# Performance work log

Measured on AMD Instinct MI355X. Metric: run time of the kernel, lower is better.

Reference implementation:

```python
import jax, jax.numpy as jnp
import numpy as np

H, NH, HD = 1024, 16, 64
WIN = 256
W = WIN // 2  # one-sided window
EXP = 4
PAD_VAL = 0.0  # pad_token_id
B, S0 = 2, 2048
NEG = float(np.finfo(np.float32).min)


def setup_inputs() -> dict:
    key = jax.random.key(0)
    ks = jax.random.split(key, 12)

    def lin(k, fi, fo):
        k1, k2 = jax.random.split(k)
        w = jax.random.normal(k1, (fi, fo), jnp.float32) / np.float32(np.sqrt(fi))
        b = jax.random.normal(k2, (fo,), jnp.float32) * 0.02
        return w, b

    x = jax.random.normal(ks[0], (B, S0, H), jnp.float32)
    mask = jnp.zeros((B, S0), jnp.int32)  # 0 = real token, 1 = pad
    wq, bq = lin(ks[1], H, H)
    wk, bk = lin(ks[2], H, H)
    wv, bv = lin(ks[3], H, H)
    wqg, bqg = lin(ks[4], H, H)
    wkg, bkg = lin(ks[5], H, H)
    wvg, bvg = lin(ks[6], H, H)
    ln_g = jnp.ones((H,), jnp.float32)
    ln_b = jnp.zeros((H,), jnp.float32)
    w1, b1 = lin(ks[7], H, H * EXP)
    w2, b2 = lin(ks[8], H * EXP, H)
    return dict(x=x, mask=mask, wq=wq, bq=bq, wk=wk, bk=bk, wv=wv, bv=bv,
                wqg=wqg, bqg=bqg, wkg=wkg, bkg=bkg, wvg=wvg, bvg=bvg,
                ln_g=ln_g, ln_b=ln_b, w1=w1, b1=b1, w2=w2, b2=b2)


def _forward(x, mask, wq, bq, wk, bk, wv, bv, wqg, bqg, wkg, bkg, wvg, bvg,
             ln_g, ln_b, w1, b1, w2, b2):
    Bsz, s0, _ = x.shape
    pad = WIN - s0 % WIN
    xp = jnp.pad(x, ((0, 0), (0, pad), (0, 0)), constant_values=PAD_VAL)
    m = jnp.pad(mask, ((0, 0), (0, pad)), constant_values=1)
    S = s0 + pad
    lm = (m * -10000).at[:, -1].set(10000)  # [B,S]; task='cls': last token global
    is_masked = lm < 0
    remove = lm != 0  # masked OR global keys removed from local windows

    inv_sqrt = np.float32(1.0 / np.sqrt(HD))
    q = ((xp @ wq + bq) * inv_sqrt).reshape(Bsz, S, NH, HD)
    k = (xp @ wk + bk).reshape(Bsz, S, NH, HD)
    v = (xp @ wv + bv).reshape(Bsz, S, NH, HD)

    nc = S // W
    # chunked banded scores: query chunk of W attends to 3W keys (prev/self/next)
    qc = q.transpose(0, 2, 1, 3).reshape(Bsz, NH, nc, W, HD)
    kpad = jnp.pad(k.transpose(0, 2, 1, 3), ((0, 0), (0, 0), (W, W), (0, 0)))
    idx3w = jnp.arange(nc)[:, None] * W + jnp.arange(3 * W)[None, :]  # [nc,3W]
    kc = kpad[:, :, idx3w]  # [B,NH,nc,3W,HD]
    sc = jnp.einsum('bhcpd,bhckd->bhcpk', qc, kc)  # [B,NH,nc,W,3W]
    p_idx = jnp.arange(W)[:, None]
    d_idx = jnp.arange(2 * W + 1)[None, :]
    band = sc[:, :, :, p_idx, p_idx + d_idx]  # [B,NH,nc,W,2W+1]
    band = band.reshape(Bsz, NH, S, 2 * W + 1).transpose(0, 2, 1, 3)  # [B,S,NH,2W+1]

    # key index j = i + d - W for offset d in [0, 2W]
    j = jnp.arange(S)[:, None] + jnp.arange(2 * W + 1)[None, :] - W
    in_range = (j >= 0) & (j < S)
    jc = jnp.clip(j, 0, S - 1)
    fmask = jnp.where(remove, NEG, 0.0)  # [B,S]
    band = band + fmask[:, jc][:, :, None, :]
    band = jnp.where(in_range[None, :, None, :], band, -jnp.inf)

    # global key column (single global token = last position), concatenated in front
    gcol = jnp.einsum('bshd,bhd->bsh', q, k[:, -1])[..., None]  # [B,S,NH,1]
    scores = jnp.concatenate([gcol, band], axis=-1)  # [B,S,NH,2W+2]
    probs = jax.nn.softmax(scores, axis=-1)
    probs = jnp.where(is_masked[:, :, None, None], 0.0, probs)

    out_g = probs[..., 0][..., None] * v[:, -1][:, None]  # [B,S,NH,HD]
    lp = probs[..., 1:].transpose(0, 2, 1, 3).reshape(Bsz, NH, nc, W, 2 * W + 1)
    pc = jnp.zeros((Bsz, NH, nc, W, 3 * W), probs.dtype).at[:, :, :, p_idx, p_idx + d_idx].set(lp)
    vpad = jnp.pad(v.transpose(0, 2, 1, 3), ((0, 0), (0, 0), (W, W), (0, 0)))
    vc = vpad[:, :, idx3w]  # [B,NH,nc,3W,HD]
    out_l = jnp.einsum('bhcpk,bhckd->bhcpd', pc, vc).reshape(Bsz, NH, S, HD).transpose(0, 2, 1, 3)
    attn = (out_l + out_g).reshape(Bsz, S, H)

    # full global attention for the global token (separate projections)
    qg = ((xp[:, -1] @ wqg + bqg) * inv_sqrt).reshape(Bsz, NH, HD)
    kg = (xp @ wkg + bkg).reshape(Bsz, S, NH, HD)
    vg = (xp @ wvg + bvg).reshape(Bsz, S, NH, HD)
    gs = jnp.einsum('bhd,bshd->bhs', qg, kg)
    gs = jnp.where(is_masked[:, None, :], NEG, gs)
    gout = jnp.einsum('bhs,bshd->bhd', jax.nn.softmax(gs, axis=-1), vg).reshape(Bsz, H)
    attn = attn.at[:, -1].set(gout)

    y = (xp + attn)[:, :s0]  # residual then strip padding
    mu = y.mean(-1, keepdims=True)
    var = ((y - mu) ** 2).mean(-1, keepdims=True)
    y = (y - mu) * jax.lax.rsqrt(var + 1e-5) * ln_g + ln_b
    h = jax.nn.gelu(y @ w1 + b1, approximate=False)
    return y + (h @ w2 + b2)


def reference(x, mask, wq, bq, wk, bk, wv, bv, wqg, bqg, wkg, bkg, wvg, bvg,
              ln_g, ln_b, w1, b1, w2, b2):
    return _forward(x, mask, wq, bq, wk, bk, wv, bv, wqg, bqg, wkg, bkg,
                    wvg, bvg, ln_g, ln_b, w1, b1, w2, b2)
```

## Files before the change

kernel.cpp:

```cpp
#include <hip/hip_runtime.h>


using bf16x8 = __attribute__((ext_vector_type(8))) short;
using bf16x4 = __attribute__((ext_vector_type(4))) short;
using f32x4  = __attribute__((ext_vector_type(4))) float;

__device__ __forceinline__ float b2f(short s) {
    return __uint_as_float(((unsigned int)(unsigned short)s) << 16);
}
__device__ __forceinline__ short f2b(float f) {
    unsigned int u = __float_as_uint(f);
    u += 0x7fffu + ((u >> 16) & 1u);
    return (short)(u >> 16);
}
__device__ __forceinline__ f32x4 mfma16(bf16x8 a, bf16x8 b, f32x4 c) {
    return __builtin_amdgcn_mfma_f32_16x16x32_bf16(a, b, c, 0, 0, 0);
}
__device__ __forceinline__ float safe_exp(float x) {
    return expf((x <= 0.f) ? x : 0.f);
}
__device__ __forceinline__ float fast_gelu(float v) {
    float z  = fabsf(v) * 0.70710678118f;
    float t  = __builtin_amdgcn_rcpf(fmaf(0.47047f, z, 1.f));
    float e  = __expf(-z * z);
    float p  = t * fmaf(t, fmaf(t, 0.7478556f, -0.0958798f), 0.3480242f);
    float er = fmaf(-p, e, 1.f);
    er = (v < 0.f) ? -er : er;
    return 0.5f * v * (1.f + er);
}
__device__ __forceinline__ void load_lds16(const short* g, short* l) {
    __builtin_amdgcn_global_load_lds((const __attribute__((address_space(1))) void*)g,
                                     (__attribute__((address_space(3))) void*)l, 16, 0, 0);
}
#define NEGF (-3.0e38f)

__global__ void cvt_f32_bf16(const float* __restrict__ in, short* __restrict__ out, int n) {
    int i = (blockIdx.x * 256 + threadIdx.x) * 4;
    f32x4 v = *(const f32x4*)(in + i);
    bf16x4 o;
#pragma unroll
    for (int j = 0; j < 4; ++j) o[j] = f2b(v[j]);
    *(bf16x4*)(out + i) = o;
}

__global__ void cvt_transpose(const float* __restrict__ in, short* __restrict__ out,
                              int R, int C) {
    __shared__ short tile[32][33];
    int bx = blockIdx.x * 32, by = blockIdx.y * 32;
    int tx = threadIdx.x, ty = threadIdx.y;
    for (int i = ty; i < 32; i += 8)
        tile[i][tx] = f2b(in[(size_t)(by + i) * C + bx + tx]);
    __syncthreads();
    for (int i = ty; i < 32; i += 8)
        out[(size_t)(bx + i) * R + by + tx] = tile[tx][i];
}

__global__ void cvt_transpose_qkv(const float* __restrict__ wq, const float* __restrict__ wk,
                                  const float* __restrict__ wv, short* __restrict__ out) {
    __shared__ short tile[32][33];
    const float* in = (blockIdx.z == 0) ? wq : (blockIdx.z == 1) ? wk : wv;
    short* dst = out + (size_t)blockIdx.z * 1024 * 1024;
    int bx = blockIdx.x * 32, by = blockIdx.y * 32;
    int tx = threadIdx.x, ty = threadIdx.y;
    for (int i = ty; i < 32; i += 8)
        tile[i][tx] = f2b(in[(size_t)(by + i) * 1024 + bx + tx]);
    __syncthreads();
    for (int i = ty; i < 32; i += 8)
        dst[(size_t)(bx + i) * 1024 + by + tx] = tile[tx][i];
}

__global__ __launch_bounds__(256, 4) void gemm_bt(
    const short* __restrict__ A, const short* __restrict__ Bt,
    const float* __restrict__ bias0, const float* __restrict__ bias1,
    const float* __restrict__ bias2,
    short* __restrict__ C, short* __restrict__ Vt,
    int M, int N, int K, float scale, int mode)
{
    __shared__ short sh[128 * 136];
    short* As = sh;
    short* Bs = sh + 8192;
    int m0 = blockIdx.x * 128, n0 = blockIdx.y * 128;
    int t = threadIdx.x;
    int wave = t >> 6, lane = t & 63, quad = lane >> 4, l16 = lane & 15;
    int wr = (wave >> 1) * 64, wc = (wave & 1) * 64;

    const short* ap[4]; const short* bp[4]; short* la[4]; short* lb[4];
    int gk = (((lane & 7) ^ (lane >> 3)) * 8);
#pragma unroll
    for (int l = 0; l < 4; ++l) {
        int c = wave * 4 + l;
        int row = c * 8 + (lane >> 3);
        ap[l] = A  + (size_t)(m0 + row) * K + gk;
        bp[l] = Bt + (size_t)(n0 + row) * K + gk;
        la[l] = As + c * 512;
        lb[l] = Bs + c * 512;
    }
    int sw = l16 & 7;

    f32x4 acc[4][4] = {};
    for (int k0 = 0; k0 < K; k0 += 64) {
#pragma unroll
        for (int l = 0; l < 4; ++l) { load_lds16(ap[l] + k0, la[l]); load_lds16(bp[l] + k0, lb[l]); }
        __syncthreads();
#pragma unroll
        for (int ks = 0; ks < 2; ++ks) {
            int slot = ((ks * 4 + quad) ^ sw) * 8;
            bf16x8 af[4], bfr[4];
#pragma unroll
            for (int i = 0; i < 4; ++i)
                af[i] = *(bf16x8*)(As + (wr + i * 16 + l16) * 64 + slot);
#pragma unroll
            for (int j = 0; j < 4; ++j)
                bfr[j] = *(bf16x8*)(Bs + (wc + j * 16 + l16) * 64 + slot);
#pragma unroll
            for (int i = 0; i < 4; ++i)
#pragma unroll
                for (int j = 0; j < 4; ++j)
                    acc[i][j] = mfma16(af[i], bfr[j], acc[i][j]);
        }
        __syncthreads();
    }

    int seg0 = n0 >> 10;
    if (mode == 1 || seg0 < 2) {
        if (mode == 1) {
#pragma unroll
            for (int j = 0; j < 4; ++j) {
                int col = n0 + wc + j * 16 + l16;
                float bs = bias0[col];
#pragma unroll
                for (int i = 0; i < 4; ++i)
#pragma unroll
                    for (int r = 0; r < 4; ++r) {
                        float v = fast_gelu(acc[i][j][r] + bs);
                        sh[(wr + i * 16 + quad * 4 + r) * 136 + wc + j * 16 + l16] = f2b(v);
                    }
            }
        } else {
            float sc = (seg0 == 0) ? scale : 1.0f;
            const float* bpt = (seg0 == 0) ? bias0 : bias1;
#pragma unroll
            for (int j = 0; j < 4; ++j) {
                int col = n0 + wc + j * 16 + l16;
                float bs = bpt[col & 1023];
#pragma unroll
                for (int i = 0; i < 4; ++i)
#pragma unroll
                    for (int r = 0; r < 4; ++r)
                        sh[(wr + i * 16 + quad * 4 + r) * 136 + wc + j * 16 + l16] =
                            f2b((acc[i][j][r] + bs) * sc);
            }
        }
        __syncthreads();
        int row = t >> 1, half = t & 1;
        const short* src = sh + row * 136 + half * 64;
        short* dst = C + (size_t)(m0 + row) * N + n0 + half * 64;
#pragma unroll
        for (int cgk = 0; cgk < 8; ++cgk)
            *(bf16x8*)(dst + cgk * 8) = *(const bf16x8*)(src + cgk * 8);
    } else {
#pragma unroll
        for (int j = 0; j < 4; ++j) {
            int cl = wc + j * 16 + l16;
            float bs = bias2[(n0 & 1023) + cl];
#pragma unroll
            for (int i = 0; i < 4; ++i)
#pragma unroll
                for (int r = 0; r < 4; ++r)
                    sh[cl * 136 + wr + i * 16 + quad * 4 + r] = f2b(acc[i][j][r] + bs);
        }
        __syncthreads();
        int h0 = (n0 & 1023) >> 6;
        int bb = m0 >> 11, s0 = m0 & 2047;
        int sc = t & 15;
#pragma unroll
        for (int cgk = 0; cgk < 8; ++cgk) {
            int cl = (t >> 4) + cgk * 16;
            int h = h0 + (cl >> 6), d = cl & 63;
            *(bf16x8*)(Vt + (((size_t)(bb * 16 + h)) * 64 + d) * 2048 + s0 + sc * 8) =
                *(const bf16x8*)(sh + cl * 136 + sc * 8);
        }
    }
}

__global__ __launch_bounds__(256, 2) void gemm128x64_db(
    const short* __restrict__ A, const short* __restrict__ Bt,
    const float* __restrict__ bias, const float* __restrict__ resf,
    float* __restrict__ Cf, int M, int N, int K)
{
    __shared__ short As[2][128 * 64];
    __shared__ short Bs[2][64 * 64];
    int m0 = blockIdx.x * 128, n0 = blockIdx.y * 64;
    int t = threadIdx.x;
    int wave = t >> 6, lane = t & 63, quad = lane >> 4, l16 = lane & 15;
    int wr = (wave >> 1) * 64, wc = (wave & 1) * 32;

    const short* ap[4]; const short* bp[2]; int loA[4], loB[2];
    int gk = (((lane & 7) ^ (lane >> 3)) * 8);
#pragma unroll
    for (int l = 0; l < 4; ++l) {
        int c = wave * 4 + l;
        int row = c * 8 + (lane >> 3);
        ap[l] = A + (size_t)(m0 + row) * K + gk;
        loA[l] = c * 512;
    }
#pragma unroll
    for (int l = 0; l < 2; ++l) {
        int c = wave * 2 + l;
        int row = c * 8 + (lane >> 3);
        bp[l] = Bt + (size_t)(n0 + row) * K + gk;
        loB[l] = c * 512;
    }
    int sw = l16 & 7;

    const int nt = K >> 6;
#pragma unroll
    for (int l = 0; l < 4; ++l) load_lds16(ap[l], &As[0][loA[l]]);
#pragma unroll
    for (int l = 0; l < 2; ++l) load_lds16(bp[l], &Bs[0][loB[l]]);

    f32x4 acc[4][2] = {};
    for (int ti = 0; ti < nt; ++ti) {
        int cur = ti & 1;
        if (ti + 1 < nt) {
            int k0 = (ti + 1) << 6;
#pragma unroll
            for (int l = 0; l < 4; ++l) load_lds16(ap[l] + k0, &As[cur ^ 1][loA[l]]);
#pragma unroll
            for (int l = 0; l < 2; ++l) load_lds16(bp[l] + k0, &Bs[cur ^ 1][loB[l]]);
            asm volatile("s_waitcnt vmcnt(6)" ::: "memory");
        } else {
            asm volatile("s_waitcnt vmcnt(0)" ::: "memory");
        }
        __builtin_amdgcn_s_barrier();
        asm volatile("" ::: "memory");

        const short* as = &As[cur][0];
        const short* bs = &Bs[cur][0];
#pragma unroll
        for (int ks = 0; ks < 2; ++ks) {
            int slot = ((ks * 4 + quad) ^ sw) * 8;
            bf16x8 af[4], bfr[2];
#pragma unroll
            for (int i = 0; i < 4; ++i)
                af[i] = *(bf16x8*)(as + (wr + i * 16 + l16) * 64 + slot);
#pragma unroll
            for (int j = 0; j < 2; ++j)
                bfr[j] = *(bf16x8*)(bs + (wc + j * 16 + l16) * 64 + slot);
#pragma unroll
            for (int i = 0; i < 4; ++i)
#pragma unroll
                for (int j = 0; j < 2; ++j)
                    acc[i][j] = mfma16(af[i], bfr[j], acc[i][j]);
        }
        asm volatile("" ::: "memory");
        __builtin_amdgcn_s_barrier();
    }

#pragma unroll
    for (int j = 0; j < 2; ++j) {
        int col = n0 + wc + j * 16 + l16;
        float bs = bias[col];
#pragma unroll
        for (int i = 0; i < 4; ++i) {
#pragma unroll
            for (int r = 0; r < 4; ++r) {
                int row = m0 + wr + i * 16 + quad * 4 + r;
                Cf[(size_t)row * N + col] = acc[i][j][r] + bs + resf[(size_t)row * N + col];
            }
        }
    }
}

__global__ __launch_bounds__(256, 2) void attn_kernel(
    const short* __restrict__ QKV, const short* __restrict__ Vt,
    const int* __restrict__ mask,
    const float* __restrict__ bk, const float* __restrict__ bv,
    short* __restrict__ attn)
{
    extern __shared__ char smem[];
    short* PsQ = (short*)smem;
    short* KV  = (short*)(smem + 34816);
    float* gkf = (float*)(smem + 53248);
    float* gvf = (float*)(smem + 53504);

    int blk = blockIdx.x;
    int c = blk & 15, h = (blk >> 4) & 15, b = blk >> 8;
    int t = threadIdx.x;
    int wave = t >> 6, lane = t & 63, quad = lane >> 4, l16 = lane & 15;
    int q0 = c * 128;
    const int bs_off = b * 2048;
    const short* Q = QKV + h * 64;
    const short* K = QKV + 1024 + h * 64;

#pragma unroll
    for (int l = 0; l < 4; ++l) {
        int idx = l * 256 + t;
        int p = idx >> 3, dc = (idx & 7) * 8;
        *(bf16x8*)(PsQ + p * 72 + dc) =
            *(const bf16x8*)(Q + ((size_t)(bs_off + q0 + p)) * 3072 + dc);
    }
    if (t < 64) { gkf[t] = bk[h * 64 + t]; gvf[t] = bv[h * 64 + t]; }
    __syncthreads();

    bf16x8 aq[2][2];
#pragma unroll
    for (int ti = 0; ti < 2; ++ti)
#pragma unroll
        for (int ks = 0; ks < 2; ++ks)
            aq[ti][ks] = *(bf16x8*)(PsQ + (wave * 32 + ti * 16 + l16) * 72 + ks * 32 + quad * 8);

    float s_g[2][4];
#pragma unroll
    for (int ti = 0; ti < 2; ++ti)
#pragma unroll
        for (int r = 0; r < 4; ++r) {
            int row = wave * 32 + ti * 16 + quad * 4 + r;
            float part = 0.f;
#pragma unroll
            for (int dd = 0; dd < 4; ++dd) {
                int d = l16 * 4 + dd;
                part += b2f(PsQ[row * 72 + d]) * gkf[d];
            }
#pragma unroll
            for (int dsh = 1; dsh < 16; dsh <<= 1) part += __shfl_xor(part, dsh);
            s_g[ti][r] = part;
        }

    f32x4 o_acc[2][4] = {};
    float m_run[2][4], l_run[2][4];
#pragma unroll
    for (int ti = 0; ti < 2; ++ti)
#pragma unroll
        for (int r = 0; r < 4; ++r) { m_run[ti][r] = NEGF; l_run[ti][r] = 0.f; }

    int kt_beg = (q0 == 0) ? 1 : 0;
    int kt_end = (q0 + 256 > 2048) ? 2 : 3;
    for (int kt = kt_beg; kt < kt_end; ++kt) {
        int jb = q0 + (kt - 1) * 128;
        __syncthreads();
#pragma unroll
        for (int l = 0; l < 4; ++l) {
            int idx = l * 256 + t;
            int p = idx >> 3, dc = (idx & 7) * 8;
            *(bf16x8*)(KV + p * 72 + dc) =
                *(const bf16x8*)(K + ((size_t)(bs_off + jb + p)) * 3072 + dc);
        }
        __syncthreads();

        f32x4 s_acc[2][8] = {};
#pragma unroll
        for (int ks = 0; ks < 2; ++ks) {
            bf16x8 bk8[8];
#pragma unroll
            for (int tj = 0; tj < 8; ++tj)
                bk8[tj] = *(bf16x8*)(KV + (tj * 16 + l16) * 72 + ks * 32 + quad * 8);
#pragma unroll
            for (int ti = 0; ti < 2; ++ti)
#pragma unroll
                for (int tj = 0; tj < 8; ++tj)
                    s_acc[ti][tj] = mfma16(aq[ti][ks], bk8[tj], s_acc[ti][tj]);
        }

        float negj[8]; int jcol[8];
#pragma unroll
        for (int tj = 0; tj < 8; ++tj) {
            jcol[tj] = jb + tj * 16 + l16;
            negj[tj] = (mask[bs_off + jcol[tj]] != 0) ? NEGF : 0.f;
        }
        float tmax[2][4];
#pragma unroll
        for (int ti = 0; ti < 2; ++ti)
#pragma unroll
            for (int r = 0; r < 4; ++r) tmax[ti][r] = NEGF;
#pragma unroll
        for (int ti = 0; ti < 2; ++ti) {
            int irow_base = q0 + wave * 32 + ti * 16 + quad * 4;
#pragma unroll
            for (int tj = 0; tj < 8; ++tj)
#pragma unroll
                for (int r = 0; r < 4; ++r) {
                    int dj = jcol[tj] - (irow_base + r);
                    float sc = (dj >= -128 && dj <= 128) ? (s_acc[ti][tj][r] + negj[tj]) : NEGF;
                    s_acc[ti][tj][r] = sc;
                    tmax[ti][r] = fmaxf(tmax[ti][r], sc);
                }
        }
#pragma unroll
        for (int ti = 0; ti < 2; ++ti)
#pragma unroll
            for (int r = 0; r < 4; ++r)
#pragma unroll
                for (int dsh = 1; dsh < 16; dsh <<= 1)
                    tmax[ti][r] = fmaxf(tmax[ti][r], __shfl_xor(tmax[ti][r], dsh));

        float alpha[2][4], lsum[2][4];
#pragma unroll
        for (int ti = 0; ti < 2; ++ti)
#pragma unroll
            for (int r = 0; r < 4; ++r) {
                float mnew = fmaxf(m_run[ti][r], tmax[ti][r]);
                alpha[ti][r] = safe_exp(m_run[ti][r] - mnew);
                m_run[ti][r] = mnew;
                lsum[ti][r] = 0.f;
            }
#pragma unroll
        for (int ti = 0; ti < 2; ++ti)
#pragma unroll
            for (int tj = 0; tj < 8; ++tj)
#pragma unroll
                for (int r = 0; r < 4; ++r) {
                    float p = safe_exp(s_acc[ti][tj][r] - m_run[ti][r]);
                    lsum[ti][r] += p;
                    PsQ[(wave * 32 + ti * 16 + quad * 4 + r) * 136 + tj * 16 + l16] = f2b(p);
                }
#pragma unroll
        for (int ti = 0; ti < 2; ++ti)
#pragma unroll
            for (int r = 0; r < 4; ++r) {
#pragma unroll
                for (int dsh = 1; dsh < 16; dsh <<= 1) lsum[ti][r] += __shfl_xor(lsum[ti][r], dsh);
                l_run[ti][r] = l_run[ti][r] * alpha[ti][r] + lsum[ti][r];
            }
#pragma unroll
        for (int ti = 0; ti < 2; ++ti)
#pragma unroll
            for (int dj = 0; dj < 4; ++dj)
#pragma unroll
                for (int r = 0; r < 4; ++r) o_acc[ti][dj][r] *= alpha[ti][r];

        __syncthreads();
#pragma unroll
        for (int l = 0; l < 4; ++l) {
            int idx = l * 256 + t;
            int d = idx >> 4, kc = (idx & 15) * 8;
            *(bf16x8*)(KV + d * 136 + kc) =
                *(const bf16x8*)(Vt + ((size_t)(b * 16 + h) * 64 + d) * 2048 + jb + kc);
        }
        __syncthreads();
#pragma unroll
        for (int ks = 0; ks < 4; ++ks) {
            bf16x8 ap[2], bv8[4];
#pragma unroll
            for (int ti = 0; ti < 2; ++ti)
                ap[ti] = *(bf16x8*)(PsQ + (wave * 32 + ti * 16 + l16) * 136 + ks * 32 + quad * 8);
#pragma unroll
            for (int dj = 0; dj < 4; ++dj)
                bv8[dj] = *(bf16x8*)(KV + (dj * 16 + l16) * 136 + ks * 32 + quad * 8);
#pragma unroll
            for (int ti = 0; ti < 2; ++ti)
#pragma unroll
                for (int dj = 0; dj < 4; ++dj)
                    o_acc[ti][dj] = mfma16(ap[ti], bv8[dj], o_acc[ti][dj]);
        }
    }

#pragma unroll
    for (int ti = 0; ti < 2; ++ti) {
        int irow_base = q0 + wave * 32 + ti * 16 + quad * 4;
#pragma unroll
        for (int r = 0; r < 4; ++r) {
            int i = irow_base + r;
            float m2 = fmaxf(m_run[ti][r], s_g[ti][r]);
            float pg = safe_exp(s_g[ti][r] - m2);
            float al = safe_exp(m_run[ti][r] - m2);
            float l2 = l_run[ti][r] * al + pg;
            float invl = 1.f / fmaxf(l2, 1e-30f);
            float qm = (mask[bs_off + i] > 0) ? 0.f : 1.f;
#pragma unroll
            for (int dj = 0; dj < 4; ++dj) {
                int d = dj * 16 + l16;
                float val = (o_acc[ti][dj][r] * al + pg * gvf[d]) * invl * qm;
                attn[((size_t)(bs_off + i)) * 1024 + h * 64 + d] = f2b(val);
            }
        }
    }
}

__global__ __launch_bounds__(256) void resid_ln(
    const float* __restrict__ x, const short* __restrict__ attn,
    const float* __restrict__ g, const float* __restrict__ be,
    short* __restrict__ yb, float* __restrict__ yf)
{
    int row = blockIdx.x, t = threadIdx.x;
    int lane = t & 63, wave = t >> 6;
    const size_t base = (size_t)row * 1024;
    float v[4]; float s = 0.f, s2 = 0.f;
#pragma unroll
    for (int i = 0; i < 4; ++i) {
        int c = i * 256 + t;
        float val = x[base + c] + b2f(attn[base + c]);
        v[i] = val; s += val; s2 += val * val;
    }
#pragma unroll
    for (int off = 32; off > 0; off >>= 1) { s += __shfl_xor(s, off); s2 += __shfl_xor(s2, off); }
    __shared__ float red[8];
    if (lane == 0) { red[wave] = s; red[4 + wave] = s2; }
    __syncthreads();
    s  = red[0] + red[1] + red[2] + red[3];
    s2 = red[4] + red[5] + red[6] + red[7];
    float mu  = s * (1.f / 1024.f);
    float var = s2 * (1.f / 1024.f) - mu * mu;
    float inv = rsqrtf(fmaxf(var, 0.f) + 1e-5f);
#pragma unroll
    for (int i = 0; i < 4; ++i) {
        int c = i * 256 + t;
        float o = (v[i] - mu) * inv * g[c] + be[c];
        yb[base + c] = f2b(o);
        yf[base + c] = o;
    }
}

static constexpr size_t MEG      = 1048576;
static constexpr size_t OFF_WQKV = 0;
static constexpr size_t OFF_W1T  = 3 * MEG;
static constexpr size_t OFF_W2T  = 7 * MEG;
static constexpr size_t OFF_XB   = 11 * MEG;
static constexpr size_t OFF_QKV  = 15 * MEG;
static constexpr size_t OFF_VT   = 27 * MEG;
static constexpr size_t OFF_ATT  = 31 * MEG;
static constexpr size_t OFF_YN   = 35 * MEG;
static constexpr size_t OFF_YF   = 39 * MEG;
static constexpr size_t OFF_H    = OFF_QKV;

extern "C" void kernel_launch(void* const* d_in, const int* in_sizes, int n_in,
                              void* d_out, int out_size, void* d_ws, size_t ws_size,
                              hipStream_t stream) {
    (void)in_sizes; (void)n_in; (void)out_size; (void)ws_size;
    const float* x    = (const float*)d_in[0];
    const int*   mask = (const int*)  d_in[1];
    const float* wq   = (const float*)d_in[2];
    const float* bq   = (const float*)d_in[3];
    const float* wk   = (const float*)d_in[4];
    const float* bk   = (const float*)d_in[5];
    const float* wv   = (const float*)d_in[6];
    const float* bv   = (const float*)d_in[7];
    const float* lng  = (const float*)d_in[14];
    const float* lnb  = (const float*)d_in[15];
    const float* w1   = (const float*)d_in[16];
    const float* b1   = (const float*)d_in[17];
    const float* w2   = (const float*)d_in[18];
    const float* b2   = (const float*)d_in[19];
    short* ws  = (short*)d_ws;
    float* out = (float*)d_out;

    dim3 tb(32, 8);
    cvt_transpose_qkv<<<dim3(32, 32, 3), tb, 0, stream>>>(wq, wk, wv, ws + OFF_WQKV);
    cvt_transpose<<<dim3(128, 32), tb, 0, stream>>>(w1, ws + OFF_W1T, 1024, 4096);
    cvt_transpose<<<dim3(32, 128), tb, 0, stream>>>(w2, ws + OFF_W2T, 4096, 1024);
    cvt_f32_bf16<<<4096, 256, 0, stream>>>(x, ws + OFF_XB, 4194304);

    gemm_bt<<<dim3(32, 24), 256, 0, stream>>>(ws + OFF_XB, ws + OFF_WQKV,
                                              bq, bk, bv,
                                              ws + OFF_QKV, ws + OFF_VT,
                                              4096, 3072, 1024, 0.125f, 0);

    attn_kernel<<<512, 256, 53760, stream>>>(ws + OFF_QKV, ws + OFF_VT,
                                             mask, bk, bv, ws + OFF_ATT);

    resid_ln<<<4096, 256, 0, stream>>>(x, ws + OFF_ATT, lng, lnb,
                                       ws + OFF_YN, (float*)(ws + OFF_YF));

    gemm_bt<<<dim3(32, 32), 256, 0, stream>>>(ws + OFF_YN, ws + OFF_W1T,
                                              b1, nullptr, nullptr,
                                              ws + OFF_H, nullptr,
                                              4096, 4096, 1024, 1.0f, 1);
    gemm128x64_db<<<dim3(32, 16), 256, 0, stream>>>(ws + OFF_H, ws + OFF_W2T,
                                                    b2, (const float*)(ws + OFF_YF),
                                                    out, 4096, 1024, 4096);
}
```

Before: 336.1 us.

## Prefetch K/V tiles into registers and use LDS-only barriers in local attention

The local attention kernel now loads the next K tile and the current V tile into registers ahead of use, so global loads overlap with the QK^T and PV MFMA work instead of stalling right before each LDS store. Full __syncthreads are replaced by a barrier that waits only on LDS counters, letting outstanding global loads stay in flight across barriers. safe_exp also switches to the fast __expf intrinsic. The prefetch adds register pressure, and only the attention kernel is affected, which is a fraction of total time dominated by GEMMs.

```diff
diff --git a/kernel.cpp b/kernel.cpp
--- a/kernel.cpp
+++ b/kernel.cpp
@@ -17,7 +17,7 @@
     return __builtin_amdgcn_mfma_f32_16x16x32_bf16(a, b, c, 0, 0, 0);
 }
 __device__ __forceinline__ float safe_exp(float x) {
-    return expf((x <= 0.f) ? x : 0.f);
+    return __expf((x <= 0.f) ? x : 0.f);
 }
 __device__ __forceinline__ float fast_gelu(float v) {
     float z  = fabsf(v) * 0.70710678118f;
@@ -31,6 +31,11 @@
 __device__ __forceinline__ void load_lds16(const short* g, short* l) {
     __builtin_amdgcn_global_load_lds((const __attribute__((address_space(1))) void*)g,
                                      (__attribute__((address_space(3))) void*)l, 16, 0, 0);
+}
+__device__ __forceinline__ void barrier_lds_only() {
+    asm volatile("s_waitcnt lgkmcnt(0)" ::: "memory");
+    __builtin_amdgcn_s_barrier();
+    asm volatile("" ::: "memory");
 }
 #define NEGF (-3.0e38f)
 
@@ -292,6 +297,7 @@
     const int bs_off = b * 2048;
     const short* Q = QKV + h * 64;
     const short* K = QKV + 1024 + h * 64;
+    const short* Vg = Vt + (size_t)(b * 16 + h) * 64 * 2048;
 
 #pragma unroll
     for (int l = 0; l < 4; ++l) {
@@ -336,17 +342,30 @@
 
     int kt_beg = (q0 == 0) ? 1 : 0;
     int kt_end = (q0 + 256 > 2048) ? 2 : 3;
+
+    bf16x8 kreg[4], vreg[4];
+    {
+        int jb = q0 + (kt_beg - 1) * 128;
+#pragma unroll
+        for (int l = 0; l < 4; ++l) {
+            int idx = l * 256 + t;
+            kreg[l] = *(const bf16x8*)(K + ((size_t)(bs_off + jb + (idx >> 3))) * 3072 + (idx & 7) * 8);
+        }
+    }
+
     for (int kt = kt_beg; kt < kt_end; ++kt) {
         int jb = q0 + (kt - 1) * 128;
-        __syncthreads();
 #pragma unroll
         for (int l = 0; l < 4; ++l) {
             int idx = l * 256 + t;
-            int p = idx >> 3, dc = (idx & 7) * 8;
-            *(bf16x8*)(KV + p * 72 + dc) =
-                *(const bf16x8*)(K + ((size_t)(bs_off + jb + p)) * 3072 + dc);
-        }
-        __syncthreads();
+            *(bf16x8*)(KV + (idx >> 3) * 72 + (idx & 7) * 8) = kreg[l];
+        }
+#pragma unroll
+        for (int l = 0; l < 4; ++l) {
+            int idx = l * 256 + t;
+            vreg[l] = *(const bf16x8*)(Vg + ((size_t)(idx >> 4)) * 2048 + jb + (idx & 15) * 8);
+        }
+        barrier_lds_only();
 
         f32x4 s_acc[2][8] = {};
 #pragma unroll
@@ -429,15 +448,23 @@
 #pragma unroll
                 for (int r = 0; r < 4; ++r) o_acc[ti][dj][r] *= alpha[ti][r];
 
-        __syncthreads();
+        barrier_lds_only();
+
 #pragma unroll
         for (int l = 0; l < 4; ++l) {
             int idx = l * 256 + t;
-            int d = idx >> 4, kc = (idx & 15) * 8;
-            *(bf16x8*)(KV + d * 136 + kc) =
-                *(const bf16x8*)(Vt + ((size_t)(b * 16 + h) * 64 + d) * 2048 + jb + kc);
-        }
-        __syncthreads();
+            *(bf16x8*)(KV + (idx >> 4) * 136 + (idx & 15) * 8) = vreg[l];
+        }
+        if (kt + 1 < kt_end) {
+            int jb2 = q0 + kt * 128;
+#pragma unroll
+            for (int l = 0; l < 4; ++l) {
+                int idx = l * 256 + t;
+                kreg[l] = *(const bf16x8*)(K + ((size_t)(bs_off + jb2 + (idx >> 3))) * 3072 + (idx & 7) * 8);
+            }
+        }
+        barrier_lds_only();
+
 #pragma unroll
         for (int ks = 0; ks < 4; ++ks) {
             bf16x8 ap[2], bv8[4];
@@ -453,6 +480,7 @@
                 for (int dj = 0; dj < 4; ++dj)
                     o_acc[ti][dj] = mfma16(ap[ti], bv8[dj], o_acc[ti][dj]);
         }
+        barrier_lds_only();
     }
 
 #pragma unroll
```

Result: faster. 316.0 us (-6.0%).
